# Optimization experiments

Hardware: AMD Instinct MI355X
Metric: run time of the kernel (lower is better)

The kernel has to match this reference:

```python
import jax, jax.numpy as jnp
import numpy as np

N, E, D, H, O, G = 50000, 800000, 64, 64, 32, 64


def setup_inputs() -> dict:
    key = jax.random.key(0)
    ks = jax.random.split(key, 12)
    x = jax.random.normal(ks[0], (N, D), dtype=jnp.float32)
    edge_index = jax.random.randint(ks[1], (2, E), 0, N)
    batch = jnp.sort(jax.random.randint(ks[2], (N,), 0, G))

    def glorot(k, fan_in, fan_out):
        s = np.sqrt(6.0 / (fan_in + fan_out)).astype(np.float32)
        return jax.random.uniform(k, (fan_in, fan_out), jnp.float32, -s, s)

    return {
        "x": x,
        "edge_index": edge_index,
        "batch": batch,
        "W1": glorot(ks[3], D, H), "b1": jnp.zeros((H,), jnp.float32),
        "W2": glorot(ks[4], H, H), "b2": jnp.zeros((H,), jnp.float32),
        "W3": glorot(ks[5], H, H), "b3": jnp.zeros((H,), jnp.float32),
        "Wl": glorot(ks[6], H, O), "bl": jnp.zeros((O,), jnp.float32),
    }


def reference(x, edge_index, batch, W1, b1, W2, b2, W3, b3, Wl, bl):
    n = x.shape[0]
    # GCNConv default: add self-loops, symmetric deg^-1/2 normalization
    loop = jnp.arange(n, dtype=edge_index.dtype)
    src = jnp.concatenate([edge_index[0], loop])  # [E+N]
    dst = jnp.concatenate([edge_index[1], loop])
    deg = jax.ops.segment_sum(jnp.ones_like(src, dtype=x.dtype), dst, num_segments=n)
    dis = jax.lax.rsqrt(deg)  # deg >= 1 due to self-loops
    norm = (dis[src] * dis[dst])[:, None]  # [E+N, 1]

    def gcn(h, W, b):
        hw = h @ W                      # [N, H] small GEMM
        msg = hw[src] * norm            # gather + scale: [E+N, H]
        agg = jax.ops.segment_sum(msg, dst, num_segments=n)  # scatter-add
        return agg + b

    h = jax.nn.relu(gcn(x, W1, b1))
    h = jax.nn.relu(gcn(h, W2, b2))
    h = gcn(h, W3, b3)

    # global_mean_pool over graph ids
    counts = jax.ops.segment_sum(jnp.ones((n,), h.dtype), batch, num_segments=G)
    pooled = jax.ops.segment_sum(h, batch, num_segments=G) / counts[:, None]

    # dropout(p=0.5) is identity in eval mode
    return pooled @ Wl + bl
```

## Files before the change

### kernel.cpp

```cpp
#include <hip/hip_runtime.h>

#define HD 64
#define PSUB 16
#define NBLK 256
#define LOG_NBLK 8
#define NBKT 512

__device__ __forceinline__ unsigned short f2bf(float f) {
    union { float f; unsigned u; } v; v.f = f;
    unsigned r = v.u + 0x7FFF + ((v.u >> 16) & 1);
    return (unsigned short)(r >> 16);
}
__device__ __forceinline__ float bf2f(unsigned short h) {
    union { unsigned u; float f; } v; v.u = ((unsigned)h) << 16;
    return v.f;
}
__device__ __forceinline__ int rdlane(int v, int l) {
    return __builtin_amdgcn_readlane(v, l);
}


__global__ __launch_bounds__(256) void hist1_k(const int* __restrict__ dst,
                                               int* __restrict__ hist, int E, int chunk)
{
    __shared__ int lh[NBKT];
    int t = threadIdx.x;
    for (int i = t; i < NBKT; i += 256) lh[i] = 0;
    __syncthreads();
    int base = blockIdx.x * chunk;
    int end  = min(base + chunk, E);
    for (int i = base + t; i < end; i += 256)
        atomicAdd(&lh[dst[i] >> 7], 1);
    __syncthreads();
    for (int i = t; i < NBKT; i += 256)
        hist[blockIdx.x * NBKT + i] = lh[i];
}

__global__ __launch_bounds__(256) void scanA_k(const int* __restrict__ hist,
                                               int* __restrict__ tsum)
{
    __shared__ int s[256];
    int t = threadIdx.x;
    int l = blockIdx.x * 256 + t;
    int phys = (l & (NBLK - 1)) * NBKT + (l >> LOG_NBLK);
    s[t] = hist[phys];
    __syncthreads();
    for (int off = 128; off > 0; off >>= 1) {
        if (t < off) s[t] += s[t + off];
        __syncthreads();
    }
    if (t == 0) tsum[blockIdx.x] = s[0];
}

__global__ __launch_bounds__(1024) void scanB_k(int* __restrict__ tsum, int nb,
    const int* __restrict__ batch, int* __restrict__ gstart, int n, int G)
{
    __shared__ int s[1024];
    int t = threadIdx.x;
    int v = (t < nb) ? tsum[t] : 0;
    s[t] = v;
    __syncthreads();
    for (int off = 1; off < 1024; off <<= 1) {
        int u = (t >= off) ? s[t - off] : 0;
        __syncthreads();
        s[t] += u;
        __syncthreads();
    }
    if (t < nb) tsum[t] = s[t] - v;
    if (t <= G) {
        if (t == G) gstart[t] = n;
        else {
            int lo = 0, hi = n;
            while (lo < hi) { int m = (lo + hi) >> 1; if (batch[m] < t) lo = m + 1; else hi = m; }
            gstart[t] = lo;
        }
    }
}

__global__ __launch_bounds__(256) void scanC_k(const int* __restrict__ hist,
                                               const int* __restrict__ tsum,
                                               int* __restrict__ scanned)
{
    __shared__ int s[256];
    int t = threadIdx.x;
    int l = blockIdx.x * 256 + t;
    int phys = (l & (NBLK - 1)) * NBKT + (l >> LOG_NBLK);
    int own = hist[phys];
    s[t] = own;
    __syncthreads();
    for (int off = 1; off < 256; off <<= 1) {
        int u = (t >= off) ? s[t - off] : 0;
        __syncthreads();
        s[t] += u;
        __syncthreads();
    }
    scanned[l] = tsum[blockIdx.x] + s[t] - own;
}

__global__ __launch_bounds__(256) void append_k(const int* __restrict__ src,
    const int* __restrict__ dst, const int* __restrict__ scanned,
    int* __restrict__ pairs, int E, int chunk)
{
    __shared__ int cur[NBKT];
    int t = threadIdx.x;
    int blk = blockIdx.x;
    for (int i = t; i < NBKT; i += 256) cur[i] = scanned[i * NBLK + blk];
    __syncthreads();
    int base = blk * chunk;
    int end  = min(base + chunk, E);
    for (int i = base + t; i < end; i += 256) {
        int s = src[i], d = dst[i];
        int p = atomicAdd(&cur[d >> 7], 1);
        pairs[p] = (s << 7) | (d & 127);
    }
}

__global__ __launch_bounds__(256) void bucket_csr_k(const int* __restrict__ pairs,
    const int* __restrict__ scanned, int* __restrict__ offsets,
    float* __restrict__ dis, int* __restrict__ csr_src, int N, int E)
{
    __shared__ int cnt[128];
    __shared__ int sc[128];
    __shared__ int cur[128];
    int t = threadIdx.x;
    int b = blockIdx.x;
    int nodeBase = b * 128;
    int nNodes = min(128, N - nodeBase);
    int bBase = scanned[b * NBLK];
    int bEnd  = (b + 1 < NBKT) ? scanned[(b + 1) * NBLK] : E;

    if (t < 128) cnt[t] = 0;
    __syncthreads();
    for (int i = bBase + t; i < bEnd; i += 256)
        atomicAdd(&cnt[pairs[i] & 127], 1);
    __syncthreads();
    int myc = (t < 128) ? cnt[t] : 0;
    if (t < 128) sc[t] = myc;
    __syncthreads();
    for (int off = 1; off < 128; off <<= 1) {
        int u = (t < 128 && t >= off) ? sc[t - off] : 0;
        __syncthreads();
        if (t < 128) sc[t] += u;
        __syncthreads();
    }
    if (t < 128) {
        int excl = sc[t] - myc;
        cur[t] = excl;
        if (t < nNodes) {
            offsets[nodeBase + t] = bBase + excl;
            dis[nodeBase + t] = rsqrtf(1.0f + (float)myc);
        }
    }
    if (t == 0 && b == gridDim.x - 1) offsets[N] = E;
    __syncthreads();
    for (int i = bBase + t; i < bEnd; i += 256) {
        int pk = pairs[i];
        int pos = bBase + atomicAdd(&cur[pk & 127], 1);
        csr_src[pos] = ((unsigned)pk) >> 7;
    }
}


__global__ __launch_bounds__(256) void gemm64_k(
    const float* __restrict__ in, const float* __restrict__ b_prev, int relu_prev,
    const float* __restrict__ W, const float* __restrict__ dis,
    unsigned short* __restrict__ outb, int n)
{
    __shared__ float HsT[HD][68];
    __shared__ float Ws[HD][HD];
    int t = threadIdx.x;
    int rowBase = blockIdx.x * 64;

    for (int i = t; i < HD * HD / 4; i += 256)
        ((float4*)Ws)[i] = ((const float4*)W)[i];

    if (blockIdx.x == 0 && t < 64)
        outb[(size_t)n * HD + t] = 0;

    {
        int k0 = (t & 15) * 4;
        float4 bb = make_float4(0.f, 0.f, 0.f, 0.f);
        if (b_prev) bb = *(const float4*)&b_prev[k0];
        for (int it = 0; it < 4; ++it) {
            int r = (t >> 4) + it * 16;
            int row = rowBase + r;
            float4 v = make_float4(0.f, 0.f, 0.f, 0.f);
            if (row < n) {
                v = *(const float4*)&in[(size_t)row * HD + k0];
                v.x += bb.x; v.y += bb.y; v.z += bb.z; v.w += bb.w;
                if (relu_prev) {
                    v.x = fmaxf(v.x, 0.f); v.y = fmaxf(v.y, 0.f);
                    v.z = fmaxf(v.z, 0.f); v.w = fmaxf(v.w, 0.f);
                }
            }
            HsT[k0 + 0][r] = v.x;
            HsT[k0 + 1][r] = v.y;
            HsT[k0 + 2][r] = v.z;
            HsT[k0 + 3][r] = v.w;
        }
    }
    __syncthreads();

    int c4 = (t & 15) * 4;
    int r4 = (t >> 4) * 4;
    float acc[4][4];
    #pragma unroll
    for (int i = 0; i < 4; ++i)
        #pragma unroll
        for (int j = 0; j < 4; ++j) acc[i][j] = 0.f;

    #pragma unroll 8
    for (int k = 0; k < HD; ++k) {
        float4 a = *(const float4*)&HsT[k][r4];
        float4 b = *(const float4*)&Ws[k][c4];
        acc[0][0] += a.x * b.x; acc[0][1] += a.x * b.y; acc[0][2] += a.x * b.z; acc[0][3] += a.x * b.w;
        acc[1][0] += a.y * b.x; acc[1][1] += a.y * b.y; acc[1][2] += a.y * b.z; acc[1][3] += a.y * b.w;
        acc[2][0] += a.z * b.x; acc[2][1] += a.z * b.y; acc[2][2] += a.z * b.z; acc[2][3] += a.z * b.w;
        acc[3][0] += a.w * b.x; acc[3][1] += a.w * b.y; acc[3][2] += a.w * b.z; acc[3][3] += a.w * b.w;
    }

    #pragma unroll
    for (int i = 0; i < 4; ++i) {
        int row = rowBase + r4 + i;
        if (row < n) {
            float ds = dis[row];
            ushort4 o;
            o.x = f2bf(ds * acc[i][0]); o.y = f2bf(ds * acc[i][1]);
            o.z = f2bf(ds * acc[i][2]); o.w = f2bf(ds * acc[i][3]);
            *(ushort4*)&outb[(size_t)row * HD + c4] = o;
        }
    }
}

__global__ __launch_bounds__(256) void agg_csr_k(const unsigned short* __restrict__ hwb,
    const float* __restrict__ dis, const int* __restrict__ offsets,
    const int* __restrict__ csr_src, float* __restrict__ agg, int n)
{
    int wid  = (blockIdx.x * blockDim.x + threadIdx.x) >> 6;
    int lane = threadIdx.x & 63;
    if (wid >= n) return;
    float acc = bf2f(hwb[(size_t)wid * HD + lane]);
    int beg = offsets[wid], end = offsets[wid + 1];

    for (int base = beg; base < end; base += 64) {
        int m = min(64, end - base);
        int idx = (lane < m) ? csr_src[base + lane] : n;
        for (int j = 0; j < m; j += 16) {
            int ss[16];
            float h[16];
            #pragma unroll
            for (int u = 0; u < 16; ++u)
                ss[u] = rdlane(idx, j + u);
            #pragma unroll
            for (int u = 0; u < 16; ++u)
                h[u] = bf2f(hwb[(size_t)ss[u] * HD + lane]);
            #pragma unroll
            for (int u = 0; u < 16; ++u)
                acc += h[u];
        }
    }
    agg[(size_t)wid * HD + lane] = dis[wid] * acc;
}

__global__ __launch_bounds__(256) void agg_pool_k(const unsigned short* __restrict__ hwb,
    const float* __restrict__ dis, const int* __restrict__ offsets,
    const int* __restrict__ csr_src, const int* __restrict__ batch,
    float* __restrict__ partial, int n)
{
    __shared__ float rows[4 * HD];
    __shared__ int   gid[4];
    int t    = threadIdx.x;
    int lane = t & 63;
    int w    = t >> 6;
    int wid  = (blockIdx.x * blockDim.x + t) >> 6;

    rows[t] = 0.f;
    if (t < 4) gid[t] = -1;

    if (wid < n) {
        float acc = bf2f(hwb[(size_t)wid * HD + lane]);
        int beg = offsets[wid], end = offsets[wid + 1];
        for (int base = beg; base < end; base += 64) {
            int m = min(64, end - base);
            int idx = (lane < m) ? csr_src[base + lane] : n;
            for (int j = 0; j < m; j += 16) {
                int ss[16];
                float h[16];
                #pragma unroll
                for (int u = 0; u < 16; ++u)
                    ss[u] = rdlane(idx, j + u);
                #pragma unroll
                for (int u = 0; u < 16; ++u)
                    h[u] = bf2f(hwb[(size_t)ss[u] * HD + lane]);
                #pragma unroll
                for (int u = 0; u < 16; ++u)
                    acc += h[u];
            }
        }
        rows[w * HD + lane] = dis[wid] * acc;
        if (lane == 0) gid[w] = batch[wid];
    }
    __syncthreads();

    if (t < HD) {
        int g0 = gid[0], g1 = gid[1], g2 = gid[2], g3 = gid[3];
        int slot = blockIdx.x & (PSUB - 1);
        if (g0 == g1 && g1 == g2 && g2 == g3 && g0 >= 0) {
            float v = rows[t] + rows[HD + t] + rows[2 * HD + t] + rows[3 * HD + t];
            atomicAdd(&partial[((size_t)g0 * PSUB + slot) * HD + t], v);
        } else {
            if (g0 >= 0) atomicAdd(&partial[((size_t)g0 * PSUB + slot) * HD + t], rows[t]);
            if (g1 >= 0) atomicAdd(&partial[((size_t)g1 * PSUB + slot) * HD + t], rows[HD + t]);
            if (g2 >= 0) atomicAdd(&partial[((size_t)g2 * PSUB + slot) * HD + t], rows[2 * HD + t]);
            if (g3 >= 0) atomicAdd(&partial[((size_t)g3 * PSUB + slot) * HD + t], rows[3 * HD + t]);
        }
    }
}

__global__ __launch_bounds__(64) void pool2_k(const float* __restrict__ partial,
    const int* __restrict__ gstart, const float* __restrict__ b3,
    const float* __restrict__ Wl, const float* __restrict__ bl,
    float* __restrict__ out, int O)
{
    __shared__ float pooled[HD];
    int g = blockIdx.x;
    int t = threadIdx.x;
    float sum = 0.0f;
    #pragma unroll
    for (int s = 0; s < PSUB; ++s)
        sum += partial[((size_t)g * PSUB + s) * HD + t];
    float cnt = (float)(gstart[g + 1] - gstart[g]);
    pooled[t] = sum / cnt + b3[t];
    __syncthreads();
    if (t < O) {
        float acc = bl[t];
        #pragma unroll
        for (int k = 0; k < HD; ++k) acc += pooled[k] * Wl[k * O + t];
        out[g * O + t] = acc;
    }
}

extern "C" void kernel_launch(void* const* d_in, const int* in_sizes, int n_in,
                              void* d_out, int out_size, void* d_ws, size_t ws_size,
                              hipStream_t stream)
{
    const float* x    = (const float*)d_in[0];
    const int*   ei   = (const int*)d_in[1];
    const int*   batch= (const int*)d_in[2];
    const float* W1   = (const float*)d_in[3];
    const float* b1   = (const float*)d_in[4];
    const float* W2   = (const float*)d_in[5];
    const float* b2   = (const float*)d_in[6];
    const float* W3   = (const float*)d_in[7];
    const float* b3   = (const float*)d_in[8];
    const float* Wl   = (const float*)d_in[9];
    const float* bl   = (const float*)d_in[10];
    float* out = (float*)d_out;

    const int N = in_sizes[0] / HD;
    const int E = in_sizes[1] / 2;
    const int O = in_sizes[10];
    const int G = out_size / O;

    const int* src = ei;
    const int* dst = ei + E;

    char* p = (char*)d_ws;
    auto take = [&](size_t bytes) { char* r = p; p += (bytes + 255) & ~(size_t)255; return r; };
    int*   csr_src = (int*)  take((size_t)(E + 256) * 4);
    int*   offsets = (int*)  take((size_t)(N + 1) * 4);
    float* dis     = (float*)take((size_t)N * 4);
    int*   gstart  = (int*)  take((size_t)(G + 1) * 4);
    float* partial = (float*)take((size_t)G * PSUB * HD * 4);
    float* aggF    = (float*)take((size_t)N * HD * 4);
    unsigned short* hwb = (unsigned short*)take((size_t)(N + 1) * HD * 2);

    int* hist    = (int*)aggF;
    int* scanned = hist + NBLK * NBKT;
    int* tsum    = scanned + NBLK * NBKT;
    int* pairs   = (int*)hwb;

    const int TB = 256;
    int chunk   = (E + NBLK - 1) / NBLK;
    int ntiles  = (NBLK * NBKT) / 256;
    int nb_gemm = (N + 63) / 64;
    int nb_agg  = (N * 64 + TB - 1) / TB;
    int nbuck   = (N + 127) / 128;

    hipMemsetAsync(partial, 0, (size_t)G * PSUB * HD * 4, stream);

    hist1_k<<<NBLK, TB, 0, stream>>>(dst, hist, E, chunk);
    scanA_k<<<ntiles, TB, 0, stream>>>(hist, tsum);
    scanB_k<<<1, 1024, 0, stream>>>(tsum, ntiles, batch, gstart, N, G);
    scanC_k<<<ntiles, TB, 0, stream>>>(hist, tsum, scanned);
    append_k<<<NBLK, TB, 0, stream>>>(src, dst, scanned, pairs, E, chunk);
    bucket_csr_k<<<nbuck, TB, 0, stream>>>(pairs, scanned, offsets, dis, csr_src, N, E);

    gemm64_k<<<nb_gemm, TB, 0, stream>>>(x, nullptr, 0, W1, dis, hwb, N);
    agg_csr_k<<<nb_agg, TB, 0, stream>>>(hwb, dis, offsets, csr_src, aggF, N);

    gemm64_k<<<nb_gemm, TB, 0, stream>>>(aggF, b1, 1, W2, dis, hwb, N);
    agg_csr_k<<<nb_agg, TB, 0, stream>>>(hwb, dis, offsets, csr_src, aggF, N);

    gemm64_k<<<nb_gemm, TB, 0, stream>>>(aggF, b2, 1, W3, dis, hwb, N);
    agg_pool_k<<<nb_agg, TB, 0, stream>>>(hwb, dis, offsets, csr_src, batch, partial, N);

    pool2_k<<<G, 64, 0, stream>>>(partial, gstart, b3, Wl, bl, out, O);
}
```

Baseline: 229.4 us.

## Fuse CSR build kernels into one persistent kernel with grid barriers

```diff
diff --git a/kernel.cpp b/kernel.cpp
--- a/kernel.cpp
+++ b/kernel.cpp
@@ -5,6 +5,7 @@
 #define NBLK 256
 #define LOG_NBLK 8
 #define NBKT 512
+#define GRID_BUILD 1024
 
 __device__ __forceinline__ unsigned short f2bf(float f) {
     union { float f; unsigned u; } v; v.f = f;
@@ -19,144 +20,150 @@
     return __builtin_amdgcn_readlane(v, l);
 }
 
-
-__global__ __launch_bounds__(256) void hist1_k(const int* __restrict__ dst,
-                                               int* __restrict__ hist, int E, int chunk)
-{
-    __shared__ int lh[NBKT];
-    int t = threadIdx.x;
-    for (int i = t; i < NBKT; i += 256) lh[i] = 0;
+__device__ __forceinline__ void gbar(int* ctr, int target) {
     __syncthreads();
-    int base = blockIdx.x * chunk;
-    int end  = min(base + chunk, E);
-    for (int i = base + t; i < end; i += 256)
-        atomicAdd(&lh[dst[i] >> 7], 1);
+    if (threadIdx.x == 0) {
+        __hip_atomic_fetch_add(ctr, 1, __ATOMIC_ACQ_REL, __HIP_MEMORY_SCOPE_AGENT);
+        while (__hip_atomic_load(ctr, __ATOMIC_ACQUIRE, __HIP_MEMORY_SCOPE_AGENT) < target)
+            __builtin_amdgcn_s_sleep(2);
+    }
     __syncthreads();
-    for (int i = t; i < NBKT; i += 256)
-        hist[blockIdx.x * NBKT + i] = lh[i];
-}
-
-__global__ __launch_bounds__(256) void scanA_k(const int* __restrict__ hist,
-                                               int* __restrict__ tsum)
-{
-    __shared__ int s[256];
-    int t = threadIdx.x;
-    int l = blockIdx.x * 256 + t;
-    int phys = (l & (NBLK - 1)) * NBKT + (l >> LOG_NBLK);
-    s[t] = hist[phys];
-    __syncthreads();
-    for (int off = 128; off > 0; off >>= 1) {
-        if (t < off) s[t] += s[t + off];
-        __syncthreads();
-    }
-    if (t == 0) tsum[blockIdx.x] = s[0];
-}
-
-__global__ __launch_bounds__(1024) void scanB_k(int* __restrict__ tsum, int nb,
-    const int* __restrict__ batch, int* __restrict__ gstart, int n, int G)
-{
-    __shared__ int s[1024];
-    int t = threadIdx.x;
-    int v = (t < nb) ? tsum[t] : 0;
-    s[t] = v;
-    __syncthreads();
-    for (int off = 1; off < 1024; off <<= 1) {
-        int u = (t >= off) ? s[t - off] : 0;
-        __syncthreads();
-        s[t] += u;
-        __syncthreads();
-    }
-    if (t < nb) tsum[t] = s[t] - v;
-    if (t <= G) {
-        if (t == G) gstart[t] = n;
-        else {
-            int lo = 0, hi = n;
-            while (lo < hi) { int m = (lo + hi) >> 1; if (batch[m] < t) lo = m + 1; else hi = m; }
-            gstart[t] = lo;
-        }
-    }
-}
-
-__global__ __launch_bounds__(256) void scanC_k(const int* __restrict__ hist,
-                                               const int* __restrict__ tsum,
-                                               int* __restrict__ scanned)
-{
-    __shared__ int s[256];
-    int t = threadIdx.x;
-    int l = blockIdx.x * 256 + t;
-    int phys = (l & (NBLK - 1)) * NBKT + (l >> LOG_NBLK);
-    int own = hist[phys];
-    s[t] = own;
-    __syncthreads();
-    for (int off = 1; off < 256; off <<= 1) {
-        int u = (t >= off) ? s[t - off] : 0;
-        __syncthreads();
-        s[t] += u;
-        __syncthreads();
-    }
-    scanned[l] = tsum[blockIdx.x] + s[t] - own;
-}
-
-__global__ __launch_bounds__(256) void append_k(const int* __restrict__ src,
-    const int* __restrict__ dst, const int* __restrict__ scanned,
-    int* __restrict__ pairs, int E, int chunk)
-{
-    __shared__ int cur[NBKT];
-    int t = threadIdx.x;
-    int blk = blockIdx.x;
-    for (int i = t; i < NBKT; i += 256) cur[i] = scanned[i * NBLK + blk];
-    __syncthreads();
-    int base = blk * chunk;
-    int end  = min(base + chunk, E);
-    for (int i = base + t; i < end; i += 256) {
-        int s = src[i], d = dst[i];
-        int p = atomicAdd(&cur[d >> 7], 1);
-        pairs[p] = (s << 7) | (d & 127);
-    }
-}
-
-__global__ __launch_bounds__(256) void bucket_csr_k(const int* __restrict__ pairs,
-    const int* __restrict__ scanned, int* __restrict__ offsets,
-    float* __restrict__ dis, int* __restrict__ csr_src, int N, int E)
-{
-    __shared__ int cnt[128];
-    __shared__ int sc[128];
-    __shared__ int cur[128];
-    int t = threadIdx.x;
-    int b = blockIdx.x;
-    int nodeBase = b * 128;
-    int nNodes = min(128, N - nodeBase);
-    int bBase = scanned[b * NBLK];
-    int bEnd  = (b + 1 < NBKT) ? scanned[(b + 1) * NBLK] : E;
-
-    if (t < 128) cnt[t] = 0;
-    __syncthreads();
-    for (int i = bBase + t; i < bEnd; i += 256)
-        atomicAdd(&cnt[pairs[i] & 127], 1);
-    __syncthreads();
-    int myc = (t < 128) ? cnt[t] : 0;
-    if (t < 128) sc[t] = myc;
-    __syncthreads();
-    for (int off = 1; off < 128; off <<= 1) {
-        int u = (t < 128 && t >= off) ? sc[t - off] : 0;
-        __syncthreads();
-        if (t < 128) sc[t] += u;
-        __syncthreads();
-    }
-    if (t < 128) {
-        int excl = sc[t] - myc;
-        cur[t] = excl;
-        if (t < nNodes) {
-            offsets[nodeBase + t] = bBase + excl;
-            dis[nodeBase + t] = rsqrtf(1.0f + (float)myc);
-        }
-    }
-    if (t == 0 && b == gridDim.x - 1) offsets[N] = E;
-    __syncthreads();
-    for (int i = bBase + t; i < bEnd; i += 256) {
-        int pk = pairs[i];
-        int pos = bBase + atomicAdd(&cur[pk & 127], 1);
-        csr_src[pos] = ((unsigned)pk) >> 7;
+}
+
+__global__ __launch_bounds__(256, 4) void build_k(
+    const int* __restrict__ src, const int* __restrict__ dst,
+    const int* __restrict__ batch,
+    int* __restrict__ hist, int* __restrict__ tsum, int* __restrict__ scanned,
+    int* __restrict__ pairs, int* __restrict__ offsets, float* __restrict__ dis,
+    int* __restrict__ csr_src, int* __restrict__ gstart,
+    float* __restrict__ partial, int psz, int* __restrict__ ctr,
+    int N, int E, int G, int chunk, int ntiles, int nbuck)
+{
+    __shared__ int lds[1024];
+    int t  = threadIdx.x;
+    int b  = blockIdx.x;
+    int nb = gridDim.x;
+
+    if (b < NBLK) {
+        for (int i = t; i < NBKT; i += 256) lds[i] = 0;
+        __syncthreads();
+        int base = b * chunk, end = min(base + chunk, E);
+        for (int i = base + t; i < end; i += 256)
+            atomicAdd(&lds[dst[i] >> 7], 1);
+        __syncthreads();
+        for (int i = t; i < NBKT; i += 256)
+            hist[b * NBKT + i] = lds[i];
+    }
+    gbar(ctr, nb * 1);
+
+    if (b < ntiles) {
+        int l = b * 256 + t;
+        int phys = (l & (NBLK - 1)) * NBKT + (l >> LOG_NBLK);
+        lds[t] = hist[phys];
+        __syncthreads();
+        for (int off = 128; off > 0; off >>= 1) {
+            if (t < off) lds[t] += lds[t + off];
+            __syncthreads();
+        }
+        if (t == 0) tsum[b] = lds[0];
+    }
+    gbar(ctr, nb * 2);
+
+    if (b == 0) {
+        int a0 = (2 * t     < ntiles) ? tsum[2 * t]     : 0;
+        int a1 = (2 * t + 1 < ntiles) ? tsum[2 * t + 1] : 0;
+        int p = a0 + a1;
+        lds[t] = p;
+        __syncthreads();
+        for (int off = 1; off < 256; off <<= 1) {
+            int u = (t >= off) ? lds[t - off] : 0;
+            __syncthreads();
+            lds[t] += u;
+            __syncthreads();
+        }
+        int exclp = lds[t] - p;
+        if (2 * t     < ntiles) tsum[2 * t]     = exclp;
+        if (2 * t + 1 < ntiles) tsum[2 * t + 1] = exclp + a0;
+    } else if (b == 1) {
+        if (t <= G) {
+            if (t == G) gstart[t] = N;
+            else {
+                int lo = 0, hi = N;
+                while (lo < hi) { int m = (lo + hi) >> 1; if (batch[m] < t) lo = m + 1; else hi = m; }
+                gstart[t] = lo;
+            }
+        }
+    } else {
+        for (int i = (b - 2) * 256 + t; i < psz; i += (nb - 2) * 256) partial[i] = 0.f;
+    }
+    gbar(ctr, nb * 3);
+
+    if (b < ntiles) {
+        int l = b * 256 + t;
+        int phys = (l & (NBLK - 1)) * NBKT + (l >> LOG_NBLK);
+        int own = hist[phys];
+        lds[t] = own;
+        __syncthreads();
+        for (int off = 1; off < 256; off <<= 1) {
+            int u = (t >= off) ? lds[t - off] : 0;
+            __syncthreads();
+            lds[t] += u;
+            __syncthreads();
+        }
+        scanned[l] = tsum[b] + lds[t] - own;
+    }
+    gbar(ctr, nb * 4);
+
+    if (b < NBLK) {
+        for (int i = t; i < NBKT; i += 256) lds[i] = scanned[i * NBLK + b];
+        __syncthreads();
+        int base = b * chunk, end = min(base + chunk, E);
+        for (int i = base + t; i < end; i += 256) {
+            int s = src[i], d = dst[i];
+            int pz = atomicAdd(&lds[d >> 7], 1);
+            pairs[pz] = (s << 7) | (d & 127);
+        }
+    }
+    gbar(ctr, nb * 5);
+
+    if (b < nbuck) {
+        int* cnt = lds;
+        int* sc  = lds + 128;
+        int* cur = lds + 256;
+        int nodeBase = b * 128;
+        int nNodes = min(128, N - nodeBase);
+        int bBase = scanned[b * NBLK];
+        int bEnd  = (b + 1 < NBKT) ? scanned[(b + 1) * NBLK] : E;
+
+        if (t < 128) cnt[t] = 0;
+        __syncthreads();
+        for (int i = bBase + t; i < bEnd; i += 256)
+            atomicAdd(&cnt[pairs[i] & 127], 1);
+        __syncthreads();
+        int myc = (t < 128) ? cnt[t] : 0;
+        if (t < 128) sc[t] = myc;
+        __syncthreads();
+        for (int off = 1; off < 128; off <<= 1) {
+            int u = (t < 128 && t >= off) ? sc[t - off] : 0;
+            __syncthreads();
+            if (t < 128) sc[t] += u;
+            __syncthreads();
+        }
+        if (t < 128) {
+            int excl = sc[t] - myc;
+            cur[t] = excl;
+            if (t < nNodes) {
+                offsets[nodeBase + t] = bBase + excl;
+                dis[nodeBase + t] = rsqrtf(1.0f + (float)myc);
+            }
+        }
+        if (t == 0 && b == nbuck - 1) offsets[N] = E;
+        __syncthreads();
+        for (int i = bBase + t; i < bEnd; i += 256) {
+            int pk = pairs[i];
+            int pos = bBase + atomicAdd(&cur[pk & 127], 1);
+            csr_src[pos] = ((unsigned)pk) >> 7;
+        }
     }
 }
 
@@ -371,6 +378,7 @@
     int*   offsets = (int*)  take((size_t)(N + 1) * 4);
     float* dis     = (float*)take((size_t)N * 4);
     int*   gstart  = (int*)  take((size_t)(G + 1) * 4);
+    int*   ctr     = (int*)  take(256);
     float* partial = (float*)take((size_t)G * PSUB * HD * 4);
     float* aggF    = (float*)take((size_t)N * HD * 4);
     unsigned short* hwb = (unsigned short*)take((size_t)(N + 1) * HD * 2);
@@ -386,15 +394,12 @@
     int nb_gemm = (N + 63) / 64;
     int nb_agg  = (N * 64 + TB - 1) / TB;
     int nbuck   = (N + 127) / 128;
-
-    hipMemsetAsync(partial, 0, (size_t)G * PSUB * HD * 4, stream);
-
-    hist1_k<<<NBLK, TB, 0, stream>>>(dst, hist, E, chunk);
-    scanA_k<<<ntiles, TB, 0, stream>>>(hist, tsum);
-    scanB_k<<<1, 1024, 0, stream>>>(tsum, ntiles, batch, gstart, N, G);
-    scanC_k<<<ntiles, TB, 0, stream>>>(hist, tsum, scanned);
-    append_k<<<NBLK, TB, 0, stream>>>(src, dst, scanned, pairs, E, chunk);
-    bucket_csr_k<<<nbuck, TB, 0, stream>>>(pairs, scanned, offsets, dis, csr_src, N, E);
+    int psz     = G * PSUB * HD;
+
+    hipMemsetAsync(ctr, 0, 4, stream);
+    build_k<<<GRID_BUILD, TB, 0, stream>>>(src, dst, batch, hist, tsum, scanned,
+        pairs, offsets, dis, csr_src, gstart, partial, psz, ctr,
+        N, E, G, chunk, ntiles, nbuck);
 
     gemm64_k<<<nb_gemm, TB, 0, stream>>>(x, nullptr, 0, W1, dis, hwb, N);
     agg_csr_k<<<nb_agg, TB, 0, stream>>>(hwb, dis, offsets, csr_src, aggF, N);
```

After: 755.1 us. +229.2%, slower.
